# Kernel optimization log

Measured on AMD Instinct MI355X. Metric: run time of the kernel, lower is better.

## Reference

```python
import jax, jax.numpy as jnp
import numpy as np


def setup_inputs() -> dict:
    key = jax.random.key(0)
    k1, k2, k3 = jax.random.split(key, 3)
    RAW_NODES = 40962          # ico-6 sphere
    NUM_NODES = RAW_NODES * 4 - 6   # 163842, ico-7 sphere
    FEAT = 256
    x = jax.random.normal(k1, (RAW_NODES, FEAT), dtype=jnp.float32)
    max_index = jax.random.randint(k2, (RAW_NODES, FEAT), 0, 7, dtype=jnp.int64)
    neigh_orders = jax.random.randint(k3, (RAW_NODES * 7,), 0, NUM_NODES, dtype=jnp.int64)
    return {"x": x, "max_index": max_index, "neigh_orders": neigh_orders, "num_nodes": NUM_NODES}


def reference(x, max_index, neigh_orders, num_nodes):
    raw_nodes, feat_num = x.shape
    # column_ref[i, f] = i*7 + max_index[i, f]  (vectorized form of the python loop)
    column_ref = (jnp.arange(raw_nodes, dtype=max_index.dtype)[:, None] * 7 + max_index).reshape(-1)
    column_index = neigh_orders[column_ref]  # gather from neighborhood lookup table
    # row_index exactly as in the original: floor(linspace(0, feat_num, raw_nodes*feat_num)), last clamped
    row_index = np.floor(np.linspace(0.0, float(feat_num), num=raw_nodes * feat_num)).astype(np.int64)
    row_index[-1] = row_index[-1] - 1
    row_index = jnp.asarray(row_index)
    y = jnp.zeros((num_nodes, feat_num), dtype=x.dtype)
    # scatter: y[column_index, row_index] = x.view(-1)
    y = y.at[column_index, row_index].set(x.reshape(-1))
    return y
```

## Files before the change

kernel.cpp:

```cpp
#include <hip/hip_runtime.h>
#include <stdint.h>


#define FEAT 256
#define LOG2FEAT 8
#define BLOCK 256
#define ROW_WGS 256
#define ZERO_WGS 1024
#define HASH 2048
#define LOG2HASH 11

extern "C" __global__ __launch_bounds__(BLOCK)
void row_build_zero_kernel(const int*   __restrict__ mi,
                           const int*   __restrict__ neigh,
                           const float* __restrict__ x,
                           float*       __restrict__ out,
                           int2*        __restrict__ winners,
                           int total,
                           int out_elems)
{
    const int tid = threadIdx.x;

    if (blockIdx.x >= ROW_WGS) {
        const int zid = blockIdx.x - ROW_WGS;
        float4* out4 = (float4*)out;
        const int total4 = out_elems >> 2;
        const float4 z = make_float4(0.f, 0.f, 0.f, 0.f);
        for (int idx = zid * BLOCK + tid; idx < total4; idx += ZERO_WGS * BLOCK)
            out4[idx] = z;
        return;
    }

    __shared__ int hkey[HASH];
    __shared__ int hval[HASH];

    for (int s = tid; s < HASH; s += BLOCK) { hkey[s] = -1; hval[s] = 0; }
    __syncthreads();

    const int r = blockIdx.x;
    const unsigned tm1 = (unsigned)(total - 1);
    const unsigned klo = ((unsigned)r * tm1 + 255u) >> 8;
    const unsigned khi = (r == 255) ? (unsigned)(total - 1)
                       : (((unsigned)(r + 1) * tm1 + 255u) >> 8) - 1u;
    const int i0 = (int)(klo >> 8);
    const int i1 = (int)(khi >> 8);

    const int lane = tid & 63;
    const int wv   = tid >> 6;

    int p0 = 0, p1 = 0, p2 = 0, p3 = 0;
    {
        const int ifirst = i0 + wv;
        if (ifirst <= i1) {
            const int* mrow = mi + (ifirst << LOG2FEAT);
            p0 = mrow[lane];       p1 = mrow[64 + lane];
            p2 = mrow[128 + lane]; p3 = mrow[192 + lane];
        }
    }

    for (int i = i0 + wv; i <= i1; i += 4) {
        const int m0 = p0, m1 = p1, m2 = p2, m3 = p3;
        const int inx = i + 4;
        if (inx <= i1) {
            const int* mrow = mi + (inx << LOG2FEAT);
            p0 = mrow[lane];       p1 = mrow[64 + lane];
            p2 = mrow[128 + lane]; p3 = mrow[192 + lane];
        }
        const int mycol = (lane < 7) ? neigh[i * 7 + lane] : 0;

        const int kbase = i << LOG2FEAT;
        int wlo = (int)klo - kbase; if (wlo < 0)   wlo = 0;
        int whi = (int)khi - kbase; if (whi > 255) whi = 255;

        unsigned long long wm[4];
        #pragma unroll
        for (int j = 0; j < 4; ++j) {
            int lo = wlo - j * 64;  if (lo < 0) lo = 0;
            int hi = whi - j * 64 + 1;
            unsigned long long mhi = (hi >= 64) ? ~0ull
                                   : (hi <= 0)  ? 0ull : ((1ull << hi) - 1ull);
            unsigned long long mlo = (lo >= 64) ? ~0ull : ((1ull << lo) - 1ull);
            wm[j] = mhi & ~mlo;
        }

        unsigned long long b[4][7];
        #pragma unroll
        for (int m = 0; m < 7; ++m) {
            b[0][m] = __ballot(m0 == m);
            b[1][m] = __ballot(m1 == m);
            b[2][m] = __ballot(m2 == m);
            b[3][m] = __ballot(m3 == m);
        }

        if (lane < 7) {
            const int m = lane;
            int bestf = -1;
            #pragma unroll
            for (int j = 3; j >= 0; --j) {
                if (bestf < 0) {
                    unsigned long long s =
                        (m == 0) ? b[j][0] : (m == 1) ? b[j][1] :
                        (m == 2) ? b[j][2] : (m == 3) ? b[j][3] :
                        (m == 4) ? b[j][4] : (m == 5) ? b[j][5] : b[j][6];
                    unsigned long long t = s & wm[j];
                    if (t) bestf = j * 64 + 63 - __clzll(t);
                }
            }
            if (bestf >= 0) {
                const int kp1 = kbase + bestf + 1;
                int slot = mycol & (HASH - 1);
                while (true) {
                    int prev = atomicCAS(&hkey[slot], -1, mycol);
                    if (prev == -1 || prev == mycol) {
                        atomicMax(&hval[slot], kp1);
                        break;
                    }
                    slot = (slot + 1) & (HASH - 1);
                }
            }
        }
    }

    __syncthreads();

    for (int s = tid; s < HASH; s += BLOCK) {
        const int key = hkey[s];
        int2 w = make_int2(-1, 0);
        if (key >= 0) {
            const int kp1 = hval[s];
            w.x = (key << LOG2FEAT) | r;
            w.y = __float_as_int(x[kp1 - 1]);
        }
        winners[(r << LOG2HASH) + s] = w;
    }
}

extern "C" __global__ __launch_bounds__(256)
void scatter_kernel(int* __restrict__ out_i,
                    const int2* __restrict__ winners,
                    int nslots)
{
    for (int idx = blockIdx.x * 256 + threadIdx.x; idx < nslots;
         idx += gridDim.x * 256) {
        const int2 w = winners[idx];
        if (w.x >= 0) out_i[w.x] = w.y;
    }
}

extern "C" void kernel_launch(void* const* d_in, const int* in_sizes, int n_in,
                              void* d_out, int out_size, void* d_ws, size_t ws_size,
                              hipStream_t stream) {
    const float* x     = (const float*)d_in[0];
    const int*   mi    = (const int*)d_in[1];
    const int*   neigh = (const int*)d_in[2];
    float*       out   = (float*)d_out;

    const int total     = in_sizes[0];
    const int out_elems = out_size;

    int2* winners = (int2*)d_ws;

    row_build_zero_kernel<<<dim3(ROW_WGS + ZERO_WGS), dim3(BLOCK), 0, stream>>>(
        mi, neigh, x, out, winners, total, out_elems);
    scatter_kernel<<<dim3(1024), dim3(256), 0, stream>>>(
        (int*)out, winners, ROW_WGS * HASH);
}
```

Before: 285.3 us.

## Replace zero-fill plus scatter with per-node bucket table and row composition

```diff
diff --git a/kernel.cpp b/kernel.cpp
--- a/kernel.cpp
+++ b/kernel.cpp
@@ -6,34 +6,32 @@
 #define LOG2FEAT 8
 #define BLOCK 256
 #define ROW_WGS 256
-#define ZERO_WGS 1024
 #define HASH 2048
 #define LOG2HASH 11
 
+typedef float f32x4 __attribute__((ext_vector_type(4)));
+
 extern "C" __global__ __launch_bounds__(BLOCK)
-void row_build_zero_kernel(const int*   __restrict__ mi,
-                           const int*   __restrict__ neigh,
-                           const float* __restrict__ x,
-                           float*       __restrict__ out,
-                           int2*        __restrict__ winners,
-                           int total,
-                           int out_elems)
+void zero_counts_kernel(int* __restrict__ count, int n)
 {
-    const int tid = threadIdx.x;
+    for (int idx = blockIdx.x * BLOCK + threadIdx.x; idx < n;
+         idx += gridDim.x * BLOCK)
+        count[idx] = 0;
+}
 
-    if (blockIdx.x >= ROW_WGS) {
-        const int zid = blockIdx.x - ROW_WGS;
-        float4* out4 = (float4*)out;
-        const int total4 = out_elems >> 2;
-        const float4 z = make_float4(0.f, 0.f, 0.f, 0.f);
-        for (int idx = zid * BLOCK + tid; idx < total4; idx += ZERO_WGS * BLOCK)
-            out4[idx] = z;
-        return;
-    }
-
+extern "C" __global__ __launch_bounds__(BLOCK)
+void row_build_kernel(const int*   __restrict__ mi,
+                      const int*   __restrict__ neigh,
+                      const float* __restrict__ x,
+                      int2*        __restrict__ table,
+                      int*         __restrict__ count,
+                      int total,
+                      int cap)
+{
     __shared__ int hkey[HASH];
     __shared__ int hval[HASH];
 
+    const int tid = threadIdx.x;
     for (int s = tid; s < HASH; s += BLOCK) { hkey[s] = -1; hval[s] = 0; }
     __syncthreads();
 
@@ -125,25 +123,49 @@
 
     for (int s = tid; s < HASH; s += BLOCK) {
         const int key = hkey[s];
-        int2 w = make_int2(-1, 0);
         if (key >= 0) {
-            const int kp1 = hval[s];
-            w.x = (key << LOG2FEAT) | r;
-            w.y = __float_as_int(x[kp1 - 1]);
+            const int kp1  = hval[s];
+            const int bits = __float_as_int(x[kp1 - 1]);
+            const int slot = atomicAdd(&count[key], 1);
+            if (slot < cap)
+                table[(size_t)key * cap + slot] = make_int2(r, bits);
         }
-        winners[(r << LOG2HASH) + s] = w;
     }
 }
 
-extern "C" __global__ __launch_bounds__(256)
-void scatter_kernel(int* __restrict__ out_i,
-                    const int2* __restrict__ winners,
-                    int nslots)
+extern "C" __global__ __launch_bounds__(BLOCK)
+void compose_kernel(float*      __restrict__ out,
+                    const int2* __restrict__ table,
+                    const int*  __restrict__ count,
+                    int nnodes, int cap)
 {
-    for (int idx = blockIdx.x * 256 + threadIdx.x; idx < nslots;
-         idx += gridDim.x * 256) {
-        const int2 w = winners[idx];
-        if (w.x >= 0) out_i[w.x] = w.y;
+    const int lane   = threadIdx.x & 63;
+    const int wv     = (blockIdx.x * BLOCK + threadIdx.x) >> 6;
+    const int nwaves = gridDim.x * (BLOCK / 64);
+
+    for (int n = wv; n < nnodes; n += nwaves) {
+        int c = count[n];
+        if (c > cap) c = cap;
+        int2 e = make_int2(-1, 0);
+        if (lane < c) e = table[(size_t)n * cap + lane];
+
+        int f0 = 0, f1 = 0, f2 = 0, f3 = 0;
+        for (int j = 0; j < c; ++j) {
+            const int rj = __shfl(e.x, j);
+            const int bj = __shfl(e.y, j);
+            if ((rj >> 2) == lane) {
+                const int q = rj & 3;
+                if      (q == 0) f0 = bj;
+                else if (q == 1) f1 = bj;
+                else if (q == 2) f2 = bj;
+                else             f3 = bj;
+            }
+        }
+        f32x4 f;
+        f.x = __int_as_float(f0); f.y = __int_as_float(f1);
+        f.z = __int_as_float(f2); f.w = __int_as_float(f3);
+        f32x4* dst = (f32x4*)(out + ((size_t)n << LOG2FEAT)) + lane;
+        __builtin_nontemporal_store(f, dst);
     }
 }
 
@@ -155,13 +177,22 @@
     const int*   neigh = (const int*)d_in[2];
     float*       out   = (float*)d_out;
 
-    const int total     = in_sizes[0];
-    const int out_elems = out_size;
+    const int total  = in_sizes[0];
+    const int nnodes = out_size >> LOG2FEAT;
 
-    int2* winners = (int2*)d_ws;
+    int cap = 32;
+    while (cap > 8 &&
+           (size_t)nnodes * (size_t)cap * sizeof(int2) + (size_t)nnodes * 4
+               > ws_size)
+        cap >>= 1;
 
-    row_build_zero_kernel<<<dim3(ROW_WGS + ZERO_WGS), dim3(BLOCK), 0, stream>>>(
-        mi, neigh, x, out, winners, total, out_elems);
-    scatter_kernel<<<dim3(1024), dim3(256), 0, stream>>>(
-        (int*)out, winners, ROW_WGS * HASH);
+    int2* table = (int2*)d_ws;
+    int*  count = (int*)((char*)d_ws +
+                         (size_t)nnodes * (size_t)cap * sizeof(int2));
+
+    zero_counts_kernel<<<dim3(512), dim3(BLOCK), 0, stream>>>(count, nnodes);
+    row_build_kernel<<<dim3(ROW_WGS), dim3(BLOCK), 0, stream>>>(
+        mi, neigh, x, table, count, total, cap);
+    compose_kernel<<<dim3(2048), dim3(BLOCK), 0, stream>>>(
+        out, table, count, nnodes, cap);
 }
```

New measurement: 306.8 us. +7.5%, slower.
